# Performance work log

Measured on AMD Instinct MI355X. Metric: run time of the kernel, lower is better.

Reference implementation:

```python
import jax, jax.numpy as jnp
import numpy as np

B, T, C, H, D, E, K = 4, 1024, 1024, 16, 64, 8, 2
HID = 2 * D  # expert MLP hidden width (assumed 2*head_dim)
NEG = jnp.finfo(jnp.float32).min


def setup_inputs() -> dict:
    key = jax.random.key(0)
    ks = jax.random.split(key, 16)
    s = 0.02
    # rotary tables [max_pos, head_dim]
    inv_freq = 1.0 / (10000.0 ** (jnp.arange(0, D, 2, dtype=jnp.float32) / D))
    freqs = jnp.arange(T, dtype=jnp.float32)[:, None] * inv_freq[None, :]
    emb = jnp.concatenate([freqs, freqs], axis=-1)  # [T, D]
    return {
        "x": jax.random.normal(ks[0], (B, T, C), jnp.float32),
        "position_ids": jnp.sort(jax.random.randint(ks[1], (B, T), 0, T), axis=-1),
        "cos": jnp.cos(emb),
        "sin": jnp.sin(emb),
        "rq": s * jax.random.normal(ks[2], (D, E), jnp.float32),
        "rk": s * jax.random.normal(ks[3], (D, E), jnp.float32),
        "rv": s * jax.random.normal(ks[4], (D, E), jnp.float32),
        "q_w1": s * jax.random.normal(ks[5], (E, D, HID), jnp.float32),
        "q_w2": s * jax.random.normal(ks[6], (E, HID, D), jnp.float32),
        "k_w1": s * jax.random.normal(ks[7], (E, D, HID), jnp.float32),
        "k_w2": s * jax.random.normal(ks[8], (E, HID, D), jnp.float32),
        "v_w1": s * jax.random.normal(ks[9], (E, D, HID), jnp.float32),
        "v_w2": s * jax.random.normal(ks[10], (E, HID, D), jnp.float32),
        "o_w": s * jax.random.normal(ks[11], (C, C), jnp.float32),  # torch Linear weight [out,in]
    }


def _rotate_half(x):
    x1, x2 = x[..., : D // 2], x[..., D // 2:]
    return jnp.concatenate([-x2, x1], axis=-1)


def _moe_head_proj(xh, r_w, w1, w2):
    """Per-head top-k routed expert MLP. xh: [B,T,H,D]."""
    logits = jnp.einsum('bthd,de->bthe', xh, r_w)            # router logits
    vals, idx = jax.lax.top_k(logits, K)                     # [B,T,H,K]
    w = jax.nn.softmax(vals, axis=-1)
    onehot = jax.nn.one_hot(idx, E, dtype=xh.dtype)          # [B,T,H,K,E]
    w_full = jnp.einsum('bthk,bthke->bthe', w, onehot)       # scatter weights to all experts
    h = jax.nn.gelu(jnp.einsum('bthd,edf->bthef', xh, w1))   # all-expert hidden
    out = jnp.einsum('bthe,bthef,efg->bthg', w_full, h, w2)  # masked weighted combine
    return out, logits


def reference(x, position_ids, cos, sin, rq, rk, rv, q_w1, q_w2, k_w1, k_w2, v_w1, v_w2, o_w):
    xh = x.reshape(B, T, H, D)
    q, _ = _moe_head_proj(xh, rq, q_w1, q_w2)
    k, _ = _moe_head_proj(xh, rk, k_w1, k_w2)
    v, _ = _moe_head_proj(xh, rv, v_w1, v_w2)
    q = q.transpose(0, 2, 1, 3)  # [B,H,T,D]
    k = k.transpose(0, 2, 1, 3)
    v = v.transpose(0, 2, 1, 3)
    # RoPE
    c = cos[position_ids][:, None, :, :]  # [B,1,T,D]
    s = sin[position_ids][:, None, :, :]
    q = q * c + _rotate_half(q) * s
    k = k * c + _rotate_half(k) * s
    # causal SDPA
    scores = jnp.einsum('bhqd,bhkd->bhqk', q, k) / jnp.sqrt(jnp.float32(D))
    causal = jnp.tril(jnp.ones((T, T), dtype=bool))
    scores = jnp.where(causal, scores, NEG)
    attn = jax.nn.softmax(scores, axis=-1)
    out = jnp.einsum('bhqk,bhkd->bhqd', attn, v)
    out = out.transpose(0, 2, 1, 3).reshape(B, T, C)
    return out @ o_w.T
```

## Files before the change

### kernel.cpp

```cpp
#include <hip/hip_runtime.h>
#include <math.h>

#define BB 4
#define TT 1024
#define CCH 1024
#define HH 16
#define DD 64
#define EE 8
#define HID 128
#define CAP 8192
#define GEXP 504

typedef unsigned short u16;
typedef unsigned int u32;
typedef short bf16x8 __attribute__((ext_vector_type(8)));
typedef short bf16x4 __attribute__((ext_vector_type(4)));
typedef float f32x4 __attribute__((ext_vector_type(4)));

__device__ __forceinline__ u16 f2bf(float f) {
    unsigned int u = __float_as_uint(f);
    unsigned int r = (u + 0x7FFFu + ((u >> 16) & 1u)) >> 16;
    return (u16)r;
}
__device__ __forceinline__ u16 f2bf_f(float f) {
    return (u16)((__float_as_uint(f) + 0x8000u) >> 16);
}
__device__ __forceinline__ u32 pkbf(float lo, float hi) {
    u32 a = __float_as_uint(lo) + 0x8000u;
    u32 b = __float_as_uint(hi) + 0x8000u;
    return __builtin_amdgcn_perm(b, a, 0x07060302u);
}
__device__ __forceinline__ float gelu_fast(float z) {
    float t = z * z;
    float wn = __builtin_fmaf(t, -0.07135481283f, -1.5957691216f);
    float e = __expf(z * wn);
    return __fdividef(z, 1.f + e);
}

#define GLD16(gp, lp) __builtin_amdgcn_global_load_lds( \
    (const __attribute__((address_space(1))) u32*)(gp), \
    (__attribute__((address_space(3))) u32*)(lp), 16, 0, 0)

__global__ __launch_bounds__(256) void prep_kernel(
    const float* __restrict__ x,
    const float* __restrict__ rq, const float* __restrict__ rk, const float* __restrict__ rv,
    unsigned int* __restrict__ counts,
    unsigned int* __restrict__ idxbuf, float2* __restrict__ wtbuf,
    const float* __restrict__ qw1, const float* __restrict__ kw1, const float* __restrict__ vw1,
    const float* __restrict__ qw2, const float* __restrict__ kw2, const float* __restrict__ vw2,
    u16* __restrict__ img1, u16* __restrict__ img2,
    const float* __restrict__ ow, u16* __restrict__ owbf)
{
    const int bi = blockIdx.x;
    const int tid = threadIdx.x;

    if (bi < 192) {
        int t = bi * 256 + tid;
        if (t < 24576) {
            int c = t & 7, f = (t >> 3) & 127, e = (t >> 10) & 7, p = t >> 13;
            const float* w1 = ((p == 0) ? qw1 : (p == 1) ? kw1 : vw1) + e * 8192;
            int dbase = 8 * (c ^ (f & 7));
            u16 tmp[8];
            #pragma unroll
            for (int j = 0; j < 8; ++j) tmp[j] = f2bf(w1[(dbase + j) * 128 + f]);
            uint4 ov;
            ov.x = (u32)tmp[0] | ((u32)tmp[1] << 16);
            ov.y = (u32)tmp[2] | ((u32)tmp[3] << 16);
            ov.z = (u32)tmp[4] | ((u32)tmp[5] << 16);
            ov.w = (u32)tmp[6] | ((u32)tmp[7] << 16);
            ((uint4*)img1)[t] = ov;
        } else {
            int i = t - 24576;
            int m = i & 15, g = (i >> 4) & 63, e = (i >> 10) & 7, p = i >> 13;
            const float* w2 = ((p == 0) ? qw2 : (p == 1) ? kw2 : vw2) + e * 8192;
            u16* dstrow = img2 + (p * 8 + e) * 8192 + g * 128;
            #pragma unroll
            for (int u = 0; u < 2; ++u) {
                int gg = 2 * m + u;
                int fbase = 16 * (gg >> 2) + 4 * (gg & 3);
                int pos = gg ^ (g & 31);
                u16 a0 = f2bf(w2[(fbase + 0) * 64 + g]);
                u16 a1 = f2bf(w2[(fbase + 1) * 64 + g]);
                u16 a2 = f2bf(w2[(fbase + 2) * 64 + g]);
                u16 a3 = f2bf(w2[(fbase + 3) * 64 + g]);
                uint2 ov;
                ov.x = (u32)a0 | ((u32)a1 << 16);
                ov.y = (u32)a2 | ((u32)a3 << 16);
                *(uint2*)(dstrow + pos * 4) = ov;
            }
        }
        return;
    }

    if (bi < 1216) {
        int i = (bi - 192) * 256 + tid;
        float4 v = ((const float4*)ow)[i];
        unsigned int lov = (unsigned int)f2bf(v.x) | ((unsigned int)f2bf(v.y) << 16);
        unsigned int hiv = (unsigned int)f2bf(v.z) | ((unsigned int)f2bf(v.w) << 16);
        ((uint2*)owbf)[i] = make_uint2(lov, hiv);
        return;
    }

    {
        const unsigned int g = (bi - 1216) * 256 + tid;

        __shared__ float rS[3][64][8];
        __shared__ int lcnt[192];
        __shared__ int lbase[192];

        for (int i = tid; i < 1536; i += 256) {
            int p = i >> 9, rem = i & 511;
            const float* rp = (p == 0) ? rq : (p == 1) ? rk : rv;
            rS[p][rem >> 3][rem & 7] = rp[rem];
        }
        if (tid < 192) lcnt[tid] = 0;
        __syncthreads();

        float lg[3][8];
        #pragma unroll
        for (int p = 0; p < 3; ++p)
            #pragma unroll
            for (int e = 0; e < 8; ++e) lg[p][e] = 0.f;

        const float* xr = x + (size_t)g * 64;
        for (int i4 = 0; i4 < 16; ++i4) {
            float4 xv = ((const float4*)xr)[i4];
            float xa[4] = {xv.x, xv.y, xv.z, xv.w};
            #pragma unroll
            for (int m = 0; m < 4; ++m) {
                int d = i4 * 4 + m;
                #pragma unroll
                for (int p = 0; p < 3; ++p) {
                    float4 r0 = *(const float4*)&rS[p][d][0];
                    float4 r1 = *(const float4*)&rS[p][d][4];
                    lg[p][0] += xa[m] * r0.x; lg[p][1] += xa[m] * r0.y;
                    lg[p][2] += xa[m] * r0.z; lg[p][3] += xa[m] * r0.w;
                    lg[p][4] += xa[m] * r1.x; lg[p][5] += xa[m] * r1.y;
                    lg[p][6] += xa[m] * r1.z; lg[p][7] += xa[m] * r1.w;
                }
            }
        }

        int ppe[3]; float2 pw[3]; int slot[3];
        #pragma unroll
        for (int p = 0; p < 3; ++p) {
            int i1 = 0; float v1 = lg[p][0];
            #pragma unroll
            for (int e = 1; e < 8; ++e) { if (lg[p][e] > v1) { v1 = lg[p][e]; i1 = e; } }
            int i2 = -1; float v2 = -3.402823466e38f;
            #pragma unroll
            for (int e = 0; e < 8; ++e) { if (e != i1 && lg[p][e] > v2) { v2 = lg[p][e]; i2 = e; } }
            float z = __expf(v2 - v1);
            float inv = 1.f / (1.f + z);
            float wa = inv, wb = z * inv;
            int lo = min(i1, i2), hi = max(i1, i2);
            float wlo = (i1 < i2) ? wa : wb;
            float whi = (i1 < i2) ? wb : wa;
            int pel = p * 64 + lo * 8 + hi;
            ppe[p] = pel; pw[p] = make_float2(wlo, whi);
            slot[p] = atomicAdd(&lcnt[pel], 1);
        }
        __syncthreads();
        if (tid < 192) {
            int c = lcnt[tid];
            lbase[tid] = c ? (int)atomicAdd(&counts[tid], (unsigned int)c) : 0;
        }
        __syncthreads();
        #pragma unroll
        for (int p = 0; p < 3; ++p) {
            int pos = lbase[ppe[p]] + slot[p];
            if (pos < CAP) {
                idxbuf[ppe[p] * CAP + pos] = g;
                wtbuf[ppe[p] * CAP + pos]  = pw[p];
            }
        }
    }
}

__global__ __launch_bounds__(128) void sched_kernel(
    const unsigned int* __restrict__ counts, unsigned int* __restrict__ blockinfo)
{
    const int tid = threadIdx.x;
    __shared__ int nsub[84];
    __shared__ int extra[84];
    __shared__ int frac[84];
    __shared__ int alloc[84];
    __shared__ int startS[84];
    __shared__ int nnzS, totalS, rem2S;

    if (tid < 84) {
        int p = tid / 28, q = tid - 28 * p, lo = 0;
        while (q >= 7 - lo) { q -= 7 - lo; ++lo; }
        int hi = lo + 1 + q;
        int n = (int)counts[p * 64 + lo * 8 + hi];
        if (n > CAP) n = CAP;
        nsub[tid] = (n + 31) >> 5;
    }
    __syncthreads();
    if (tid == 0) {
        int tot = 0, nz = 0;
        for (int i = 0; i < 84; ++i) { tot += nsub[i]; nz += (nsub[i] > 0); }
        totalS = tot; nnzS = nz;
    }
    __syncthreads();
    const int R = GEXP - nnzS;
    if (tid < 84) {
        if (nsub[tid] > 0) {
            int e = (int)(((long long)nsub[tid] * R) / totalS);
            extra[tid] = e;
            frac[tid] = nsub[tid] * R - e * totalS;
        } else { extra[tid] = 0; frac[tid] = -1; }
    }
    __syncthreads();
    if (tid == 0) {
        int se = 0;
        for (int i = 0; i < 84; ++i) se += extra[i];
        rem2S = GEXP - nnzS - se;
    }
    __syncthreads();
    if (tid < 84) {
        if (nsub[tid] > 0) {
            int rank = 0;
            for (int j = 0; j < 84; ++j)
                if (nsub[j] > 0 && (frac[j] > frac[tid] || (frac[j] == frac[tid] && j < tid))) ++rank;
            alloc[tid] = 1 + extra[tid] + (rank < rem2S ? 1 : 0);
        } else alloc[tid] = 0;
    }
    __syncthreads();
    if (tid == 0) {
        int s = 0;
        for (int i = 0; i < 84; ++i) { startS[i] = s; s += alloc[i]; }
    }
    __syncthreads();
    if (tid < 84) {
        int a = alloc[tid], st = startS[tid];
        for (int c = 0; c < a; ++c)
            blockinfo[st + c] = (unsigned)tid | ((unsigned)c << 8) | ((unsigned)a << 20);
    }
}

__global__ __launch_bounds__(512, 2) void expert_kernel(
    const float* __restrict__ x, const int* __restrict__ pos_ids,
    const float* __restrict__ cosb, const float* __restrict__ sinb,
    const u16* __restrict__ img1, const u16* __restrict__ img2,
    const unsigned int* __restrict__ counts,
    const unsigned int* __restrict__ idxbuf, const float2* __restrict__ wtbuf,
    const unsigned int* __restrict__ blockinfo,
    u16* __restrict__ qb, u16* __restrict__ kb, u16* __restrict__ vb)
{
    const int tid = threadIdx.x;
    const unsigned int info = blockinfo[blockIdx.x];
    const int pe84 = info & 255;
    const int chunk = (info >> 8) & 0xFFF;
    const int nch = info >> 20;
    const int p = pe84 / 28;
    int q28 = pe84 - p * 28;
    int lo = 0;
    while (q28 >= 7 - lo) { q28 -= 7 - lo; ++lo; }
    const int hi = lo + 1 + q28;
    const int pe = p * 64 + lo * 8 + hi;

    int n = (int)counts[pe]; if (n == 0) return; if (n > CAP) n = CAP;

    u16* outp = (p == 0) ? qb : (p == 1) ? kb : vb;
    const unsigned int* il = idxbuf + pe * CAP;
    const float2* wl = wtbuf + pe * CAP;

    __shared__ __align__(16) u16 wsh[32768];

    {
        const u16* a0 = img1 + (p * 8 + lo) * 8192;
        const u16* b0 = img2 + (p * 8 + lo) * 8192;
        const u16* a1 = img1 + (p * 8 + hi) * 8192;
        const u16* b1 = img2 + (p * 8 + hi) * 8192;
        #pragma unroll
        for (int k = 0; k < 2; ++k) {
            int o = (k * 512 + tid) * 8;
            GLD16(a0 + o, wsh + o);
            GLD16(b0 + o, wsh + 8192 + o);
            GLD16(a1 + o, wsh + 16384 + o);
            GLD16(b1 + o, wsh + 24576 + o);
        }
    }
    __syncthreads();

    const int lane = tid & 63, w = tid >> 6, quad = lane >> 4, m16 = lane & 15;
    const int f7 = m16 & 7;
    const int wid = chunk * 8 + w;
    const int WRK = nch * 8;
    const int nsub = (n + 31) >> 5;

    for (int s = wid; s < nsub; s += WRK) {
        const int base = s * 32;
        unsigned int gtok = 0, obase = 0; float wlo_ = 0.f, whi_ = 0.f;
        int posv = 0, valid = 0;
        if (lane < 32) {
            int j = base + lane;
            valid = (j < n);
            int jc = valid ? j : (n - 1);
            gtok = il[jc];
            float2 wv = wl[jc];
            wlo_ = valid ? wv.x : 0.f; whi_ = valid ? wv.y : 0.f;
            unsigned int b_ = gtok >> 14, h_ = gtok & 15, t_ = (gtok >> 4) & 1023;
            obase = ((b_ * 16 + h_) * 1024 + t_) * 64;
            posv = pos_ids[b_ * 1024 + t_];
        }

        float wf00 = __shfl(wlo_, m16, 64);
        float wf10 = __shfl(whi_, m16, 64);
        float wf01 = __shfl(wlo_, 16 + m16, 64);
        float wf11 = __shfl(whi_, 16 + m16, 64);

        bf16x8 Afr[2][2];
        #pragma unroll
        for (int mt2 = 0; mt2 < 2; ++mt2) {
            unsigned int gm = (unsigned int)__shfl((int)gtok, mt2 * 16 + m16, 64);
            const float* xr = x + (size_t)gm * 64 + 8 * quad;
            float4 xa0 = *(const float4*)(xr);
            float4 xa1 = *(const float4*)(xr + 4);
            float4 xb0 = *(const float4*)(xr + 32);
            float4 xb1 = *(const float4*)(xr + 36);
            bf16x8 A0, A1;
            A0[0] = (short)f2bf_f(xa0.x); A0[1] = (short)f2bf_f(xa0.y);
            A0[2] = (short)f2bf_f(xa0.z); A0[3] = (short)f2bf_f(xa0.w);
            A0[4] = (short)f2bf_f(xa1.x); A0[5] = (short)f2bf_f(xa1.y);
            A0[6] = (short)f2bf_f(xa1.z); A0[7] = (short)f2bf_f(xa1.w);
            A1[0] = (short)f2bf_f(xb0.x); A1[1] = (short)f2bf_f(xb0.y);
            A1[2] = (short)f2bf_f(xb0.z); A1[3] = (short)f2bf_f(xb0.w);
            A1[4] = (short)f2bf_f(xb1.x); A1[5] = (short)f2bf_f(xb1.y);
            A1[6] = (short)f2bf_f(xb1.z); A1[7] = (short)f2bf_f(xb1.w);
            Afr[mt2][0] = A0; Afr[mt2][1] = A1;
        }

        f32x4 acc2[2][4];
        #pragma unroll
        for (int mt2 = 0; mt2 < 2; ++mt2)
            #pragma unroll
            for (int nt = 0; nt < 4; ++nt) acc2[mt2][nt] = (f32x4){0.f, 0.f, 0.f, 0.f};

        #pragma unroll 1
        for (int ekk = 0; ekk < 8; ++ekk) {
            const int e = ekk >> 2;
            const int kk = ekk & 3;
            const u16* w1b = wsh + e * 16384;
            const u16* w2b = w1b + 8192;
            const float wt0 = e ? wf10 : wf00;
            const float wt1 = e ? wf11 : wf01;

            f32x4 c[2][2];
            #pragma unroll
            for (int ntl = 0; ntl < 2; ++ntl) {
                const int f = 16 * (2 * kk + ntl) + m16;
                const u16* w1f = w1b + f * 64;
                bf16x8 wa = *(const bf16x8*)(w1f + (((quad    ) ^ f7) << 3));
                bf16x8 wb = *(const bf16x8*)(w1f + (((quad + 4) ^ f7) << 3));
                #pragma unroll
                for (int mt2 = 0; mt2 < 2; ++mt2) {
                    f32x4 t = (f32x4){0.f, 0.f, 0.f, 0.f};
                    t = __builtin_amdgcn_mfma_f32_16x16x32_bf16(wa, Afr[mt2][0], t, 0, 0, 0);
                    c[ntl][mt2] = __builtin_amdgcn_mfma_f32_16x16x32_bf16(wb, Afr[mt2][1], t, 0, 0, 0);
                }
            }

            bf16x4 w2f[2][4];
            #pragma unroll
            for (int ntl = 0; ntl < 2; ++ntl) {
                const int gg = 4 * (2 * kk + ntl) + quad;
                #pragma unroll
                for (int nt2 = 0; nt2 < 4; ++nt2) {
                    const int g = 16 * nt2 + m16;
                    const int pos = gg ^ (g & 31);
                    w2f[ntl][nt2] = *(const bf16x4*)(w2b + g * 128 + pos * 4);
                }
            }

            #pragma unroll
            for (int mt2 = 0; mt2 < 2; ++mt2) {
                const float wt = mt2 ? wt1 : wt0;
                #pragma unroll
                for (int ntl = 0; ntl < 2; ++ntl) {
                    float g0 = wt * gelu_fast(c[ntl][mt2][0]);
                    float g1 = wt * gelu_fast(c[ntl][mt2][1]);
                    float g2 = wt * gelu_fast(c[ntl][mt2][2]);
                    float g3 = wt * gelu_fast(c[ntl][mt2][3]);
                    union { u32 u[2]; bf16x4 v; } bf_;
                    bf_.u[0] = pkbf(g0, g1);
                    bf_.u[1] = pkbf(g2, g3);
                    #pragma unroll
                    for (int nt2 = 0; nt2 < 4; ++nt2)
                        acc2[mt2][nt2] = __builtin_amdgcn_mfma_f32_16x16x16bf16_1k(
                            w2f[ntl][nt2], bf_.v, acc2[mt2][nt2], 0, 0, 0);
                }
            }
        }

        #pragma unroll
        for (int mt2 = 0; mt2 < 2; ++mt2) {
            const int tk = mt2 * 16 + m16;
            int   pos_r = __shfl(posv, tk, 64);
            unsigned int ob = (unsigned int)__shfl((int)obase, tk, 64);
            int   val_r = __shfl(valid, tk, 64);
            if (p < 2) {
                #pragma unroll
                for (int ntp = 0; ntp < 2; ++ntp) {
                    const int d0 = 16 * ntp + 4 * quad;
                    float4 cv = *(const float4*)&cosb[pos_r * 64 + d0];
                    float4 sv = *(const float4*)&sinb[pos_r * 64 + d0];
                    float o1[4], o2[4];
                    #pragma unroll
                    for (int r = 0; r < 4; ++r) {
                        float v1 = acc2[mt2][ntp][r];
                        float v2 = acc2[mt2][ntp + 2][r];
                        float cd = (&cv.x)[r], sd = (&sv.x)[r];
                        o1[r] = v1 * cd - v2 * sd;
                        o2[r] = v2 * cd + v1 * sd;
                    }
                    if (val_r) {
                        uint2 s1, s2;
                        s1.x = (u32)f2bf(o1[0]) | ((u32)f2bf(o1[1]) << 16);
                        s1.y = (u32)f2bf(o1[2]) | ((u32)f2bf(o1[3]) << 16);
                        s2.x = (u32)f2bf(o2[0]) | ((u32)f2bf(o2[1]) << 16);
                        s2.y = (u32)f2bf(o2[2]) | ((u32)f2bf(o2[3]) << 16);
                        *(uint2*)&outp[ob + d0]      = s1;
                        *(uint2*)&outp[ob + d0 + 32] = s2;
                    }
                }
            } else {
                if (val_r) {
                    #pragma unroll
                    for (int nt2 = 0; nt2 < 4; ++nt2) {
                        uint2 s1;
                        s1.x = (u32)f2bf(acc2[mt2][nt2][0]) | ((u32)f2bf(acc2[mt2][nt2][1]) << 16);
                        s1.y = (u32)f2bf(acc2[mt2][nt2][2]) | ((u32)f2bf(acc2[mt2][nt2][3]) << 16);
                        *(uint2*)&outp[ob + 16 * nt2 + 4 * quad] = s1;
                    }
                }
            }
        }
    }
}

__global__ __launch_bounds__(256) void attn_kernel(
    const u16* __restrict__ qbp, const u16* __restrict__ kbp,
    const u16* __restrict__ vbp, u16* __restrict__ ao)
{
    const int tid = threadIdx.x;
    const int i8 = blockIdx.x & 7;
    const int plane_i = blockIdx.x >> 3;
    const int h = plane_i & 15, b = plane_i >> 4;
    const size_t plane = (size_t)plane_i * 1024 * 64;
    const u16* qp = qbp + plane;
    const u16* kp = kbp + plane;
    const u16* vp = vbp + plane;

    const int w = tid >> 6, lane = tid & 63, quad = lane >> 4, m16 = lane & 15;
    const int row = tid >> 2, seg = tid & 3;
    const int kjv = tid & 63, dgv = tid >> 6;

    __shared__ u16 Ks[64][72];
    __shared__ u16 Vt[64][72];
    __shared__ u16 Ps[4][16][72];

    #pragma unroll 1
    for (int half = 0; half < 2; ++half) {
        const int qt = half ? (15 - i8) : i8;
        const int q0 = qt * 64;

        const u16* qrow = &qp[(size_t)(q0 + 16 * w + m16) * 64 + 8 * quad];
        bf16x8 aq0 = *(const bf16x8*)(qrow);
        bf16x8 aq1 = *(const bf16x8*)(qrow + 32);

        uint4 kr0, kr1; ushort4 vr0, vr1, vr2, vr3;
        {
            const uint4* src = (const uint4*)&kp[(size_t)row * 64 + seg * 16];
            kr0 = src[0]; kr1 = src[1];
            const u16* vb2 = &vp[(size_t)kjv * 64 + dgv * 4];
            vr0 = *(const ushort4*)(vb2);
            vr1 = *(const ushort4*)(vb2 + 16);
            vr2 = *(const ushort4*)(vb2 + 32);
            vr3 = *(const ushort4*)(vb2 + 48);
        }

        float m_r[4], l_r[4];
        #pragma unroll
        for (int i = 0; i < 4; ++i) { m_r[i] = -1e30f; l_r[i] = 0.f; }
        f32x4 oacc[4];
        #pragma unroll
        for (int i = 0; i < 4; ++i) oacc[i] = (f32x4){0.f, 0.f, 0.f, 0.f};

        for (int kt = 0; kt <= qt; ++kt) {
            __syncthreads();
            {
                uint4* dst = (uint4*)&Ks[row][seg * 16];
                dst[0] = kr0; dst[1] = kr1;
                int d0 = dgv * 4;
                Vt[d0 + 0][kjv] = vr0.x; Vt[d0 + 1][kjv] = vr0.y;
                Vt[d0 + 2][kjv] = vr0.z; Vt[d0 + 3][kjv] = vr0.w;
                Vt[d0 + 16][kjv] = vr1.x; Vt[d0 + 17][kjv] = vr1.y;
                Vt[d0 + 18][kjv] = vr1.z; Vt[d0 + 19][kjv] = vr1.w;
                Vt[d0 + 32][kjv] = vr2.x; Vt[d0 + 33][kjv] = vr2.y;
                Vt[d0 + 34][kjv] = vr2.z; Vt[d0 + 35][kjv] = vr2.w;
                Vt[d0 + 48][kjv] = vr3.x; Vt[d0 + 49][kjv] = vr3.y;
                Vt[d0 + 50][kjv] = vr3.z; Vt[d0 + 51][kjv] = vr3.w;
            }
            __syncthreads();
            if (kt < qt) {
                const int k0n = (kt + 1) * 64;
                const uint4* src = (const uint4*)&kp[(size_t)(k0n + row) * 64 + seg * 16];
                kr0 = src[0]; kr1 = src[1];
                const u16* vb2 = &vp[(size_t)(k0n + kjv) * 64 + dgv * 4];
                vr0 = *(const ushort4*)(vb2);
                vr1 = *(const ushort4*)(vb2 + 16);
                vr2 = *(const ushort4*)(vb2 + 32);
                vr3 = *(const ushort4*)(vb2 + 48);
            }

            f32x4 sv[4];
            #pragma unroll
            for (int ct = 0; ct < 4; ++ct) {
                bf16x8 bk0 = *(const bf16x8*)&Ks[16 * ct + m16][8 * quad];
                bf16x8 bk1 = *(const bf16x8*)&Ks[16 * ct + m16][32 + 8 * quad];
                f32x4 acc = (f32x4){0.f, 0.f, 0.f, 0.f};
                acc = __builtin_amdgcn_mfma_f32_16x16x32_bf16(aq0, bk0, acc, 0, 0, 0);
                acc = __builtin_amdgcn_mfma_f32_16x16x32_bf16(aq1, bk1, acc, 0, 0, 0);
                sv[ct] = acc;
            }

            float s[4][4];
            const bool diag = (kt == qt);
            #pragma unroll
            for (int ct = 0; ct < 4; ++ct)
                #pragma unroll
                for (int reg = 0; reg < 4; ++reg) {
                    float v = sv[ct][reg] * 0.125f;
                    if (diag) {
                        int col = 16 * ct + m16;
                        int rw = 16 * w + 4 * quad + reg;
                        if (col > rw) v = -1e30f;
                    }
                    s[ct][reg] = v;
                }

            float nm[4], al[4];
            #pragma unroll
            for (int reg = 0; reg < 4; ++reg) {
                float rm = fmaxf(fmaxf(s[0][reg], s[1][reg]), fmaxf(s[2][reg], s[3][reg]));
                #pragma unroll
                for (int off = 1; off < 16; off <<= 1) rm = fmaxf(rm, __shfl_xor(rm, off, 16));
                float mn = fmaxf(m_r[reg], rm);
                nm[reg] = mn;
                al[reg] = __expf(m_r[reg] - mn);
            }
            #pragma unroll
            for (int reg = 0; reg < 4; ++reg) {
                float sum = 0.f;
                #pragma unroll
                for (int ct = 0; ct < 4; ++ct) {
                    float pv = __expf(s[ct][reg] - nm[reg]);
                    s[ct][reg] = pv;
                    sum += pv;
                }
                #pragma unroll
                for (int off = 1; off < 16; off <<= 1) sum += __shfl_xor(sum, off, 16);
                l_r[reg] = l_r[reg] * al[reg] + sum;
                m_r[reg] = nm[reg];
            }

            #pragma unroll
            for (int ct = 0; ct < 4; ++ct)
                #pragma unroll
                for (int reg = 0; reg < 4; ++reg)
                    Ps[w][4 * quad + reg][16 * ct + m16] = f2bf(s[ct][reg]);

            #pragma unroll
            for (int dt = 0; dt < 4; ++dt)
                #pragma unroll
                for (int reg = 0; reg < 4; ++reg) oacc[dt][reg] *= al[reg];

            bf16x8 ap0 = *(const bf16x8*)&Ps[w][m16][8 * quad];
            bf16x8 ap1 = *(const bf16x8*)&Ps[w][m16][32 + 8 * quad];
            #pragma unroll
            for (int dt = 0; dt < 4; ++dt) {
                bf16x8 bv0 = *(const bf16x8*)&Vt[16 * dt + m16][8 * quad];
                bf16x8 bv1 = *(const bf16x8*)&Vt[16 * dt + m16][32 + 8 * quad];
                oacc[dt] = __builtin_amdgcn_mfma_f32_16x16x32_bf16(ap0, bv0, oacc[dt], 0, 0, 0);
                oacc[dt] = __builtin_amdgcn_mfma_f32_16x16x32_bf16(ap1, bv1, oacc[dt], 0, 0, 0);
            }
        }

        #pragma unroll
        for (int reg = 0; reg < 4; ++reg) {
            float linv = 1.f / l_r[reg];
            int rw = q0 + 16 * w + 4 * quad + reg;
            size_t base = ((size_t)(b * 1024) + rw) * 1024 + h * 64;
            #pragma unroll
            for (int dt = 0; dt < 4; ++dt)
                ao[base + 16 * dt + m16] = f2bf(oacc[dt][reg] * linv);
        }
    }
}

__global__ __launch_bounds__(256) void oproj_kernel(
    const u16* __restrict__ A, const u16* __restrict__ Bw,
    float* __restrict__ out)
{
    const int tid = threadIdx.x;
    const int bn = blockIdx.x & 7;
    const int bm = blockIdx.x >> 3;
    const int m0 = bm * 128, n0 = bn * 128;
    const int w = tid >> 6, lane = tid & 63, quad = lane >> 4, m16 = lane & 15;
    const int wm = (w >> 1) * 64, wn = (w & 1) * 64;

    __shared__ u16 As[128][32];
    __shared__ u16 Bs[128][32];

    f32x4 acc[4][4];
    #pragma unroll
    for (int mt = 0; mt < 4; ++mt)
        #pragma unroll
        for (int nt = 0; nt < 4; ++nt) acc[mt][nt] = (f32x4){0.f, 0.f, 0.f, 0.f};

    for (int k0 = 0; k0 < 1024; k0 += 32) {
        __syncthreads();
        {
            int rw = tid >> 1, sg = (tid & 1) * 16;
            const uint4* srcA = (const uint4*)&A[(size_t)(m0 + rw) * 1024 + k0 + sg];
            uint4 a0 = srcA[0], a1 = srcA[1];
            uint4* dstA = (uint4*)&As[rw][sg];
            dstA[0] = a0; dstA[1] = a1;
            const uint4* srcB = (const uint4*)&Bw[(size_t)(n0 + rw) * 1024 + k0 + sg];
            uint4 b0 = srcB[0], b1 = srcB[1];
            uint4* dstB = (uint4*)&Bs[rw][sg];
            dstB[0] = b0; dstB[1] = b1;
        }
        __syncthreads();
        bf16x8 af[4], bf_[4];
        #pragma unroll
        for (int mt = 0; mt < 4; ++mt) af[mt] = *(const bf16x8*)&As[wm + 16 * mt + m16][8 * quad];
        #pragma unroll
        for (int nt = 0; nt < 4; ++nt) bf_[nt] = *(const bf16x8*)&Bs[wn + 16 * nt + m16][8 * quad];
        #pragma unroll
        for (int mt = 0; mt < 4; ++mt)
            #pragma unroll
            for (int nt = 0; nt < 4; ++nt)
                acc[mt][nt] = __builtin_amdgcn_mfma_f32_16x16x32_bf16(af[mt], bf_[nt], acc[mt][nt], 0, 0, 0);
    }
    #pragma unroll
    for (int mt = 0; mt < 4; ++mt)
        #pragma unroll
        for (int nt = 0; nt < 4; ++nt)
            #pragma unroll
            for (int reg = 0; reg < 4; ++reg)
                out[(size_t)(m0 + wm + 16 * mt + 4 * quad + reg) * 1024 + n0 + wn + 16 * nt + m16] =
                    acc[mt][nt][reg];
}

extern "C" void kernel_launch(void* const* d_in, const int* in_sizes, int n_in,
                              void* d_out, int out_size, void* d_ws, size_t ws_size,
                              hipStream_t stream) {
    (void)in_sizes; (void)n_in; (void)out_size; (void)ws_size;
    const float* x    = (const float*)d_in[0];
    const int*   pid  = (const int*)  d_in[1];
    const float* cosb = (const float*)d_in[2];
    const float* sinb = (const float*)d_in[3];
    const float* rq   = (const float*)d_in[4];
    const float* rk   = (const float*)d_in[5];
    const float* rv   = (const float*)d_in[6];
    const float* qw1  = (const float*)d_in[7];
    const float* qw2  = (const float*)d_in[8];
    const float* kw1  = (const float*)d_in[9];
    const float* kw2  = (const float*)d_in[10];
    const float* vw1  = (const float*)d_in[11];
    const float* vw2  = (const float*)d_in[12];
    const float* ow   = (const float*)d_in[13];
    float* out = (float*)d_out;

    const size_t MB = 1u << 20;
    char* wsb = (char*)d_ws;
    u16* qb   = (u16*)(wsb + 0 * MB);
    u16* kb   = (u16*)(wsb + 8 * MB);
    u16* vb   = (u16*)(wsb + 16 * MB);
    u16* aobf = (u16*)(wsb + 24 * MB);
    u16* owbf = (u16*)(wsb + 32 * MB);
    unsigned int* idxbuf = (unsigned int*)(wsb + 34 * MB);
    float2*       wtbuf  = (float2*)(wsb + 41 * MB);
    unsigned int* counts = (unsigned int*)(wsb + 54 * MB);
    unsigned int* blockinfo = (unsigned int*)(wsb + 54 * MB + 4096);
    u16* w1img = (u16*)(wsb + 56 * MB);
    u16* w2img = (u16*)(wsb + 57 * MB);

    hipMemsetAsync(counts, 0, 1024, stream);

    hipLaunchKernelGGL(prep_kernel, dim3(1472), dim3(256), 0, stream,
                       x, rq, rk, rv, counts, idxbuf, wtbuf,
                       qw1, kw1, vw1, qw2, kw2, vw2, w1img, w2img,
                       ow, owbf);
    hipLaunchKernelGGL(sched_kernel, dim3(1), dim3(128), 0, stream,
                       counts, blockinfo);
    hipLaunchKernelGGL(expert_kernel, dim3(GEXP), dim3(512), 0, stream,
                       x, pid, cosb, sinb, w1img, w2img,
                       counts, idxbuf, wtbuf, blockinfo, qb, kb, vb);
    hipLaunchKernelGGL(attn_kernel, dim3(512), dim3(256), 0, stream,
                       qb, kb, vb, aobf);
    hipLaunchKernelGGL(oproj_kernel, dim3(256), dim3(256), 0, stream,
                       aobf, owbf, out);
}
```

Before: 237.8 us.

## Compute transposed S=K·Q^T so P stays in registers for PV MFMA

Swaps the MFMA operands in the QK^T product so each lane holds one query row's scores. Row max and sum then need only two cross-lane shuffles instead of per-register 16-lane reductions. The probabilities are packed directly into bf16x4 operands for 16x16x16 MFMAs against V, which removes the per-tile LDS round trip through Ps. The output is transposed through LDS once at the end. The cost is twice as many smaller MFMA instructions for the PV product and an extra barrier in the epilogue.

Result: faster. 229.2 us (-3.6%).

```diff
diff --git a/kernel.cpp b/kernel.cpp
--- a/kernel.cpp
+++ b/kernel.cpp
@@ -481,12 +481,12 @@
             vr3 = *(const ushort4*)(vb2 + 48);
         }
 
-        float m_r[4], l_r[4];
-        #pragma unroll
-        for (int i = 0; i < 4; ++i) { m_r[i] = -1e30f; l_r[i] = 0.f; }
+        float m_s = -1e30f, l_s = 0.f;
         f32x4 oacc[4];
         #pragma unroll
         for (int i = 0; i < 4; ++i) oacc[i] = (f32x4){0.f, 0.f, 0.f, 0.f};
+
+        const int qrow_l = 16 * w + m16;
 
         for (int kt = 0; kt <= qt; ++kt) {
             __syncthreads();
@@ -521,8 +521,8 @@
                 bf16x8 bk0 = *(const bf16x8*)&Ks[16 * ct + m16][8 * quad];
                 bf16x8 bk1 = *(const bf16x8*)&Ks[16 * ct + m16][32 + 8 * quad];
                 f32x4 acc = (f32x4){0.f, 0.f, 0.f, 0.f};
-                acc = __builtin_amdgcn_mfma_f32_16x16x32_bf16(aq0, bk0, acc, 0, 0, 0);
-                acc = __builtin_amdgcn_mfma_f32_16x16x32_bf16(aq1, bk1, acc, 0, 0, 0);
+                acc = __builtin_amdgcn_mfma_f32_16x16x32_bf16(bk0, aq0, acc, 0, 0, 0);
+                acc = __builtin_amdgcn_mfma_f32_16x16x32_bf16(bk1, aq1, acc, 0, 0, 0);
                 sv[ct] = acc;
             }
 
@@ -534,68 +534,75 @@
                 for (int reg = 0; reg < 4; ++reg) {
                     float v = sv[ct][reg] * 0.125f;
                     if (diag) {
-                        int col = 16 * ct + m16;
-                        int rw = 16 * w + 4 * quad + reg;
-                        if (col > rw) v = -1e30f;
+                        int krow = 16 * ct + 4 * quad + reg;
+                        if (krow > qrow_l) v = -1e30f;
                     }
                     s[ct][reg] = v;
                 }
 
-            float nm[4], al[4];
-            #pragma unroll
-            for (int reg = 0; reg < 4; ++reg) {
-                float rm = fmaxf(fmaxf(s[0][reg], s[1][reg]), fmaxf(s[2][reg], s[3][reg]));
-                #pragma unroll
-                for (int off = 1; off < 16; off <<= 1) rm = fmaxf(rm, __shfl_xor(rm, off, 16));
-                float mn = fmaxf(m_r[reg], rm);
-                nm[reg] = mn;
-                al[reg] = __expf(m_r[reg] - mn);
-            }
-            #pragma unroll
-            for (int reg = 0; reg < 4; ++reg) {
-                float sum = 0.f;
-                #pragma unroll
-                for (int ct = 0; ct < 4; ++ct) {
-                    float pv = __expf(s[ct][reg] - nm[reg]);
+            float rm = s[0][0];
+            #pragma unroll
+            for (int ct = 0; ct < 4; ++ct)
+                #pragma unroll
+                for (int reg = 0; reg < 4; ++reg) rm = fmaxf(rm, s[ct][reg]);
+            rm = fmaxf(rm, __shfl_xor(rm, 16, 64));
+            rm = fmaxf(rm, __shfl_xor(rm, 32, 64));
+            float mn = fmaxf(m_s, rm);
+            float al = __expf(m_s - mn);
+            float sum = 0.f;
+            #pragma unroll
+            for (int ct = 0; ct < 4; ++ct)
+                #pragma unroll
+                for (int reg = 0; reg < 4; ++reg) {
+                    float pv = __expf(s[ct][reg] - mn);
                     s[ct][reg] = pv;
                     sum += pv;
                 }
-                #pragma unroll
-                for (int off = 1; off < 16; off <<= 1) sum += __shfl_xor(sum, off, 16);
-                l_r[reg] = l_r[reg] * al[reg] + sum;
-                m_r[reg] = nm[reg];
-            }
-
-            #pragma unroll
-            for (int ct = 0; ct < 4; ++ct)
-                #pragma unroll
-                for (int reg = 0; reg < 4; ++reg)
-                    Ps[w][4 * quad + reg][16 * ct + m16] = f2bf(s[ct][reg]);
+            sum += __shfl_xor(sum, 16, 64);
+            sum += __shfl_xor(sum, 32, 64);
+            l_s = l_s * al + sum;
+            m_s = mn;
+
+            bf16x4 pt[4];
+            #pragma unroll
+            for (int ct = 0; ct < 4; ++ct) {
+                union { u32 u[2]; bf16x4 v; } pb;
+                pb.u[0] = pkbf(s[ct][0], s[ct][1]);
+                pb.u[1] = pkbf(s[ct][2], s[ct][3]);
+                pt[ct] = pb.v;
+            }
 
             #pragma unroll
             for (int dt = 0; dt < 4; ++dt)
                 #pragma unroll
-                for (int reg = 0; reg < 4; ++reg) oacc[dt][reg] *= al[reg];
-
-            bf16x8 ap0 = *(const bf16x8*)&Ps[w][m16][8 * quad];
-            bf16x8 ap1 = *(const bf16x8*)&Ps[w][m16][32 + 8 * quad];
+                for (int reg = 0; reg < 4; ++reg) oacc[dt][reg] *= al;
+
             #pragma unroll
             for (int dt = 0; dt < 4; ++dt) {
-                bf16x8 bv0 = *(const bf16x8*)&Vt[16 * dt + m16][8 * quad];
-                bf16x8 bv1 = *(const bf16x8*)&Vt[16 * dt + m16][32 + 8 * quad];
-                oacc[dt] = __builtin_amdgcn_mfma_f32_16x16x32_bf16(ap0, bv0, oacc[dt], 0, 0, 0);
-                oacc[dt] = __builtin_amdgcn_mfma_f32_16x16x32_bf16(ap1, bv1, oacc[dt], 0, 0, 0);
-            }
-        }
-
+                #pragma unroll
+                for (int ct = 0; ct < 4; ++ct) {
+                    bf16x4 vf = *(const bf16x4*)&Vt[16 * dt + m16][16 * ct + 4 * quad];
+                    oacc[dt] = __builtin_amdgcn_mfma_f32_16x16x16bf16_1k(vf, pt[ct], oacc[dt], 0, 0, 0);
+                }
+            }
+        }
+
+        float linv = 1.f / l_s;
+        #pragma unroll
+        for (int dt = 0; dt < 4; ++dt) {
+            u32 lo = (u32)f2bf(oacc[dt][0] * linv) | ((u32)f2bf(oacc[dt][1] * linv) << 16);
+            u32 hi = (u32)f2bf(oacc[dt][2] * linv) | ((u32)f2bf(oacc[dt][3] * linv) << 16);
+            *(u32*)&Ps[w][m16][16 * dt + 4 * quad]     = lo;
+            *(u32*)&Ps[w][m16][16 * dt + 4 * quad + 2] = hi;
+        }
+        __syncthreads();
         #pragma unroll
         for (int reg = 0; reg < 4; ++reg) {
-            float linv = 1.f / l_r[reg];
             int rw = q0 + 16 * w + 4 * quad + reg;
             size_t base = ((size_t)(b * 1024) + rw) * 1024 + h * 64;
             #pragma unroll
             for (int dt = 0; dt < 4; ++dt)
-                ao[base + 16 * dt + m16] = f2bf(oacc[dt][reg] * linv);
+                ao[base + 16 * dt + m16] = Ps[w][4 * quad + reg][16 * dt + m16];
         }
     }
 }
```
